# Kernel optimization log

Hardware: AMD Instinct MI355X
Metric: run time of the kernel (lower is better)

## Reference

```python
import jax, jax.numpy as jnp
import numpy as np

B, S, H = 4, 2048, 1024
NH, HD = 16, 64  # num heads, head dim


def setup_inputs() -> dict:
    key = jax.random.key(0)
    ks = jax.random.split(key, 8)
    s = 1.0 / np.sqrt(H)
    return {
        "hidden_states": jax.random.normal(ks[0], (B, S, H), jnp.float32),
        "attention_mask": jnp.zeros((B, 1, 1, S), jnp.float32),
        "Wq": jax.random.normal(ks[1], (H, H), jnp.float32) * s,
        "bq": jnp.zeros((H,), jnp.float32),
        "Wk": jax.random.normal(ks[2], (H, H), jnp.float32) * s,
        "bk": jnp.zeros((H,), jnp.float32),
        "Wv": jax.random.normal(ks[3], (H, H), jnp.float32) * s,
        "bv": jnp.zeros((H,), jnp.float32),
    }


def _split_heads(x):
    # [B, S, H] -> [B, NH, S, HD]
    return x.reshape(B, S, NH, HD).transpose(0, 2, 1, 3)


def reference(hidden_states, attention_mask, Wq, bq, Wk, bk, Wv, bv):
    q = _split_heads(hidden_states @ Wq + bq)
    k = _split_heads(hidden_states @ Wk + bk)
    v = _split_heads(hidden_states @ Wv + bv)
    scores = jnp.einsum("bhqd,bhkd->bhqk", q, k) / jnp.sqrt(jnp.float32(HD))
    probs = jax.nn.softmax(scores + attention_mask, axis=-1)  # dropout p=0 -> identity
    ctx = jnp.einsum("bhqk,bhkd->bhqd", probs, v)
    ctx = ctx.transpose(0, 2, 1, 3).reshape(B, S, H)
    return (ctx,)
```

## Files before the change

### kernel.cpp

```cpp
#include <hip/hip_runtime.h>
#include <hip/hip_bf16.h>
#include <stdint.h>


typedef unsigned short ushort_t;
typedef __attribute__((ext_vector_type(4))) float f32x4;
typedef __attribute__((ext_vector_type(16))) float f32x16;
typedef __attribute__((ext_vector_type(8))) short short8;

#define MFMA16(a, b, c) __builtin_amdgcn_mfma_f32_16x16x32_bf16((a), (b), (c), 0, 0, 0)
#define MFMA32(a, b, c) __builtin_amdgcn_mfma_f32_32x32x16_bf16((a), (b), (c), 0, 0, 0)

__device__ __forceinline__ ushort_t f2bf(float f) {
  unsigned u = __float_as_uint(f);
  u = (u + 0x7FFFu + ((u >> 16) & 1u)) >> 16;
  return (ushort_t)u;
}

typedef __attribute__((address_space(1))) unsigned int as1_uint;
typedef __attribute__((address_space(3))) unsigned int as3_uint;

__device__ __forceinline__ void async16(void* lds_dst, const void* g_src) {
  __builtin_amdgcn_global_load_lds((as1_uint*)(uintptr_t)g_src,
                                   (as3_uint*)(unsigned)(uintptr_t)lds_dst, 16, 0, 0);
}

__global__ __launch_bounds__(256) void convert_x(const float* __restrict__ X,
                                                 ushort_t* __restrict__ Xb) {
  int idx = (blockIdx.x * 256 + threadIdx.x) * 8;
  f32x4 a = *(const f32x4*)(X + idx);
  f32x4 b = *(const f32x4*)(X + idx + 4);
  short8 r;
#pragma unroll
  for (int j = 0; j < 4; ++j) r[j] = (short)f2bf(a[j]);
#pragma unroll
  for (int j = 0; j < 4; ++j) r[4 + j] = (short)f2bf(b[j]);
  *(short8*)(Xb + idx) = r;
}

__global__ __launch_bounds__(256) void convert_w(const float* __restrict__ Wq,
                                                 const float* __restrict__ Wk,
                                                 const float* __restrict__ Wv,
                                                 ushort_t* __restrict__ Wt) {
  const int mat = blockIdx.z;
  const float* W = (mat == 0) ? Wq : ((mat == 1) ? Wk : Wv);
  const int k0 = blockIdx.x * 64, n0 = blockIdx.y * 64;
  __shared__ float t[64][65];
  const int tid = threadIdx.x;
#pragma unroll
  for (int it = 0; it < 16; ++it) {
    int idx = it * 256 + tid;
    int r = idx >> 6, c = idx & 63;
    t[r][c] = W[(size_t)(k0 + r) * 1024 + n0 + c];
  }
  __syncthreads();
#pragma unroll
  for (int it = 0; it < 16; ++it) {
    int idx = it * 256 + tid;
    int nr = idx >> 6, kc = idx & 63;
    Wt[(size_t)(mat * 1024 + n0 + nr) * 1024 + k0 + kc] = f2bf(t[kc][nr]);
  }
}

__global__ __launch_bounds__(256) void gemm_qkv(const ushort_t* __restrict__ Xb,
                                                const ushort_t* __restrict__ Wt,
                                                const float* __restrict__ bq,
                                                const float* __restrict__ bk,
                                                const float* __restrict__ bv,
                                                ushort_t* __restrict__ Qb,
                                                ushort_t* __restrict__ Kb,
                                                ushort_t* __restrict__ Vt) {
  __shared__ char lds[36864];
  const int tid = threadIdx.x;
  const int l = tid & 63, w = tid >> 6;
  const int m0 = blockIdx.x * 128;
  const int n0 = blockIdx.y * 128;
  const int wm = w >> 1, wn = w & 1;

  const int lr = l >> 3;
  const int kb_log = (((l & 7) ^ lr) << 4);
  const char* srcA = (const char*)Xb + (size_t)(m0 + w * 32 + lr) * 2048 + kb_log;
  const char* srcB = (const char*)Wt + (size_t)(n0 + w * 32 + lr) * 2048 + kb_log;
  char* ldsA_w = lds + w * 4096;
  char* ldsB_w = lds + 16384 + w * 4096;

  const int ra = wm * 64 + (l & 15);
  const int rb = wn * 64 + (l & 15);
  const int swz = (l & 7) << 4;
  const int x0 = (((l >> 4) << 4)) ^ swz;
  const int x1 = (64 + ((l >> 4) << 4)) ^ swz;

  f32x4 acc[4][4];
#pragma unroll
  for (int mf = 0; mf < 4; ++mf)
#pragma unroll
    for (int nf = 0; nf < 4; ++nf) acc[mf][nf] = (f32x4){0.f, 0.f, 0.f, 0.f};

#pragma unroll 1
  for (int kt = 0; kt < 16; ++kt) {
    if (kt) __syncthreads();
    const int koff = kt * 128;
#pragma unroll
    for (int c = 0; c < 4; ++c) {
      async16(ldsA_w + c * 1024, srcA + c * 16384 + koff);
      async16(ldsB_w + c * 1024, srcB + c * 16384 + koff);
    }
    __syncthreads();
#pragma unroll
    for (int half = 0; half < 2; ++half) {
      const int xo = half ? x1 : x0;
      short8 av[4], bv2[4];
#pragma unroll
      for (int mf = 0; mf < 4; ++mf)
        av[mf] = *(const short8*)(lds + (ra + mf * 16) * 128 + xo);
#pragma unroll
      for (int nf = 0; nf < 4; ++nf)
        bv2[nf] = *(const short8*)(lds + 16384 + (rb + nf * 16) * 128 + xo);
#pragma unroll
      for (int mf = 0; mf < 4; ++mf)
#pragma unroll
        for (int nf = 0; nf < 4; ++nf)
          acc[mf][nf] = MFMA16(av[mf], bv2[nf], acc[mf][nf]);
    }
  }

  __syncthreads();
  const int col0 = n0 + wn * 64;
  const int mat = col0 >> 10;
  const int nn0 = col0 & 1023;
  const int hh = nn0 >> 6;
  const int row0 = m0 + wm * 64;
  const int bb = row0 >> 11;
  const int s0 = row0 & 2047;
  const float* bias = (mat == 0) ? bq : ((mat == 1) ? bk : bv);
  const float qscale = 0.18033688011112042f;
  if (mat < 2) {
    ushort_t* dst = (mat == 0) ? Qb : Kb;
    const float scl = (mat == 0) ? qscale : 1.0f;
#pragma unroll
    for (int mf = 0; mf < 4; ++mf)
#pragma unroll
      for (int nf = 0; nf < 4; ++nf)
#pragma unroll
        for (int i = 0; i < 4; ++i) {
          int r = mf * 16 + (l >> 4) * 4 + i;
          int d = nf * 16 + (l & 15);
          float v = (acc[mf][nf][i] + bias[nn0 + d]) * scl;
          dst[((size_t)(bb * 16 + hh) * 2048 + (s0 + r)) * 64 + d] = f2bf(v);
        }
  } else {
    ushort_t* vw = (ushort_t*)(lds + w * 9216);
#pragma unroll
    for (int mf = 0; mf < 4; ++mf)
#pragma unroll
      for (int nf = 0; nf < 4; ++nf)
#pragma unroll
        for (int i = 0; i < 4; ++i) {
          int r = mf * 16 + (l >> 4) * 4 + i;
          int d = nf * 16 + (l & 15);
          float v = acc[mf][nf][i] + bias[nn0 + d];
          vw[d * 72 + r] = f2bf(v);
        }
#pragma unroll
    for (int it = 0; it < 8; ++it) {
      int dr = it * 8 + (l >> 3);
      int sc = (l & 7) * 8;
      short8 vv = *(const short8*)((const char*)vw + dr * 144 + sc * 2);
      *(short8*)((char*)Vt + (((size_t)(bb * 16 + hh) * 64 + dr) * 2048 + s0 + sc) * 2) = vv;
    }
  }
}

__global__ __launch_bounds__(256, 4) void attn_fwd(const ushort_t* __restrict__ Qb,
                                                   const ushort_t* __restrict__ Kb,
                                                   const ushort_t* __restrict__ Vt,
                                                   const float* __restrict__ mask,
                                                   float* __restrict__ out) {
  __shared__ char lds[33280];
  const int tid = threadIdx.x, l = tid & 63, w = tid >> 6;
  const int bh = blockIdx.y;
  const int bb = bh >> 4, hh = bh & 15;
  const int q0 = blockIdx.x * 128;
  const int l31 = l & 31, hi = l >> 5;
  char* klds = lds;
  char* vlds = lds + 16384;
  float* sbuf = (float*)(lds + 32768) + w * 32;

  const float LOG2E = 1.44269504088896340736f;
  const int psz = (l & 7) << 4;

  const char* qrow = (const char*)Qb + ((size_t)bh * 2048 + q0 + w * 32 + l31) * 128 + hi * 16;
  short8 qf[4];
#pragma unroll
  for (int c = 0; c < 4; ++c) qf[c] = *(const short8*)(qrow + c * 32);

  const int srow = l >> 3;
  const int scol = ((l & 7) ^ srow) << 4;
  const char* ksrc0 = (const char*)Kb + (size_t)bh * 2048 * 128 + (size_t)(w * 16 + srow) * 128 + scol;
  const char* vsrc0 = (const char*)Vt + ((size_t)bh * 64 + w * 16 + srow) * 4096 + scol;

  {
    char* kd = klds + w * 2048;
    char* vd = vlds + w * 2048;
    async16(kd, ksrc0);
    async16(kd + 1024, ksrc0 + 1024);
    async16(vd, vsrc0);
    async16(vd + 1024, vsrc0 + 8 * 4096);
  }

  const float* mrow = mask + (size_t)bb * 2048;

  f32x16 o0, o1;
#pragma unroll
  for (int i = 0; i < 16; ++i) { o0[i] = 0.f; o1[i] = 0.f; }
  f32x4 lsum4 = (f32x4){0.f, 0.f, 0.f, 0.f};

#pragma unroll 1
  for (int kt = 0; kt < 32; ++kt) {
    const int cur = kt & 1;
    asm volatile("s_waitcnt lgkmcnt(0)" ::: "memory");
    __builtin_amdgcn_s_barrier();
    __builtin_amdgcn_sched_barrier(0);
    if (kt < 31) {
      char* kd = klds + (cur ^ 1) * 8192 + w * 2048;
      char* vd = vlds + (cur ^ 1) * 8192 + w * 2048;
      const char* ks = ksrc0 + (size_t)(kt + 1) * 8192;
      const char* vs = vsrc0 + (kt + 1) * 128;
      async16(kd, ks);
      async16(kd + 1024, ks + 1024);
      async16(vd, vs);
      async16(vd + 1024, vs + 8 * 4096);
      asm volatile("s_waitcnt vmcnt(4)" ::: "memory");
    } else {
      asm volatile("s_waitcnt vmcnt(0)" ::: "memory");
    }
    __builtin_amdgcn_s_barrier();
    __builtin_amdgcn_sched_barrier(0);

    const char* kbuf = klds + cur * 8192;
    const char* vbuf = vlds + cur * 8192;

#pragma unroll
    for (int kb = 0; kb < 2; ++kb) {
      f32x16 s;
#pragma unroll
      for (int i = 0; i < 16; ++i) s[i] = 0.f;
#pragma unroll
      for (int c = 0; c < 4; ++c) {
        short8 kf = *(const short8*)(kbuf + (kb * 32 + l31) * 128 + ((c * 32 + hi * 16) ^ psz));
        s = MFMA32(kf, qf[c], s);
      }
      f32x16 pp;
#pragma unroll
      for (int r2 = 0; r2 < 4; ++r2) {
        f32x4 m4 = *(const f32x4*)(mrow + kt * 64 + kb * 32 + 8 * r2 + 4 * hi);
#pragma unroll
        for (int i = 0; i < 4; ++i)
          pp[4 * r2 + i] = __builtin_amdgcn_exp2f(fmaf(m4[i], LOG2E, s[4 * r2 + i]));
      }
#pragma unroll
      for (int i = 0; i < 4; ++i)
        lsum4[i] += ((pp[i] + pp[4 + i]) + (pp[8 + i] + pp[12 + i]));

      unsigned u[8];
#pragma unroll
      for (int r2 = 0; r2 < 4; ++r2) {
        asm("v_cvt_pk_bf16_f32 %0, %1, %2"
            : "=v"(u[2 * r2]) : "v"(pp[4 * r2]), "v"(pp[4 * r2 + 1]));
        asm("v_cvt_pk_bf16_f32 %0, %1, %2"
            : "=v"(u[2 * r2 + 1]) : "v"(pp[4 * r2 + 2]), "v"(pp[4 * r2 + 3]));
      }
      short8 pa[2];
#pragma unroll
      for (int c = 0; c < 2; ++c) {
        unsigned a0 = u[4 * c], b0 = u[4 * c + 2];
        unsigned a1 = u[4 * c + 1], b1 = u[4 * c + 3];
        unsigned s0 = hi ? a0 : b0;
        unsigned s1 = hi ? a1 : b1;
        unsigned r0 = (unsigned)__shfl_xor((int)s0, 32);
        unsigned r1 = (unsigned)__shfl_xor((int)s1, 32);
        union { unsigned uu[4]; short8 s8; } cv;
        cv.uu[0] = hi ? r0 : a0;
        cv.uu[1] = hi ? r1 : a1;
        cv.uu[2] = hi ? b0 : r0;
        cv.uu[3] = hi ? b1 : r1;
        pa[c] = cv.s8;
      }

      __builtin_amdgcn_s_setprio(1);
#pragma unroll
      for (int c = 0; c < 2; ++c) {
        const int koff = (kb * 64 + c * 32 + hi * 16) ^ psz;
        short8 v0 = *(const short8*)(vbuf + l31 * 128 + koff);
        short8 v1 = *(const short8*)(vbuf + (32 + l31) * 128 + koff);
        o0 = MFMA32(pa[c], v0, o0);
        o1 = MFMA32(pa[c], v1, o1);
      }
      __builtin_amdgcn_s_setprio(0);
    }
  }

  float ls = (lsum4[0] + lsum4[1]) + (lsum4[2] + lsum4[3]);
  float other = __shfl_xor(ls, 32);
  float inv = 1.0f / (ls + other);
  if (hi == 0) sbuf[l31] = inv;
  float* obase = out + ((size_t)bb * 2048 + q0 + w * 32) * 1024 + hh * 64;
#pragma unroll
  for (int r2 = 0; r2 < 4; ++r2) {
    f32x4 iv = *(const f32x4*)(sbuf + 8 * r2 + 4 * hi);
#pragma unroll
    for (int r0 = 0; r0 < 4; ++r0) {
      const int q = 8 * r2 + 4 * hi + r0;
      obase[(size_t)q * 1024 + l31] = o0[4 * r2 + r0] * iv[r0];
      obase[(size_t)q * 1024 + 32 + l31] = o1[4 * r2 + r0] * iv[r0];
    }
  }
}

extern "C" void kernel_launch(void* const* d_in, const int* in_sizes, int n_in,
                              void* d_out, int out_size, void* d_ws, size_t ws_size,
                              hipStream_t stream) {
  const float* hs  = (const float*)d_in[0];
  const float* msk = (const float*)d_in[1];
  const float* Wq  = (const float*)d_in[2];
  const float* bq  = (const float*)d_in[3];
  const float* Wk  = (const float*)d_in[4];
  const float* bk  = (const float*)d_in[5];
  const float* Wv  = (const float*)d_in[6];
  const float* bv  = (const float*)d_in[7];
  float* out = (float*)d_out;
  char* ws = (char*)d_ws;
  ushort_t* Xb = (ushort_t*)ws;
  ushort_t* Wt = (ushort_t*)(ws + (16u << 20));
  ushort_t* Qb = (ushort_t*)(ws + (22u << 20));
  ushort_t* Kb = (ushort_t*)(ws + (38u << 20));
  ushort_t* Vt = (ushort_t*)(ws + (54u << 20));

  convert_x<<<4096, 256, 0, stream>>>(hs, Xb);
  convert_w<<<dim3(16, 16, 3), 256, 0, stream>>>(Wq, Wk, Wv, Wt);
  gemm_qkv<<<dim3(64, 24), 256, 0, stream>>>(Xb, Wt, bq, bk, bv, Qb, Kb, Vt);
  attn_fwd<<<dim3(16, 64), 256, 0, stream>>>(Qb, Kb, Vt, msk, out);
}
```

Before: 251.8 us.

## Rewrite QKV GEMM with 256x256 tiles and double-buffered async LDS pipeline

Enlarges the QKV projection GEMM tile from 128x128 with 4 waves to 256x256 with 8 waves, using a 128KB double-buffered LDS. Global-to-LDS async loads for the next K tile are interleaved with MFMA phases, using explicit waitcnt, barriers and s_setprio. The aim is to hide load latency and raise data reuse per block. In exchange, the large LDS footprint limits occupancy to one block per CU, and the 384-block grid may leave a partial last wave.

```diff
diff --git a/kernel.cpp b/kernel.cpp
--- a/kernel.cpp
+++ b/kernel.cpp
@@ -62,74 +62,154 @@
   }
 }
 
-__global__ __launch_bounds__(256) void gemm_qkv(const ushort_t* __restrict__ Xb,
-                                                const ushort_t* __restrict__ Wt,
-                                                const float* __restrict__ bq,
-                                                const float* __restrict__ bk,
-                                                const float* __restrict__ bv,
-                                                ushort_t* __restrict__ Qb,
-                                                ushort_t* __restrict__ Kb,
-                                                ushort_t* __restrict__ Vt) {
-  __shared__ char lds[36864];
+__global__ __launch_bounds__(512, 2) void gemm_qkv(const ushort_t* __restrict__ Xb,
+                                                   const ushort_t* __restrict__ Wt,
+                                                   const float* __restrict__ bq,
+                                                   const float* __restrict__ bk,
+                                                   const float* __restrict__ bv,
+                                                   ushort_t* __restrict__ Qb,
+                                                   ushort_t* __restrict__ Kb,
+                                                   ushort_t* __restrict__ Vt) {
+  __shared__ __align__(16) char lds[131072];
   const int tid = threadIdx.x;
   const int l = tid & 63, w = tid >> 6;
-  const int m0 = blockIdx.x * 128;
-  const int n0 = blockIdx.y * 128;
-  const int wm = w >> 1, wn = w & 1;
-
-  const int lr = l >> 3;
-  const int kb_log = (((l & 7) ^ lr) << 4);
-  const char* srcA = (const char*)Xb + (size_t)(m0 + w * 32 + lr) * 2048 + kb_log;
-  const char* srcB = (const char*)Wt + (size_t)(n0 + w * 32 + lr) * 2048 + kb_log;
-  char* ldsA_w = lds + w * 4096;
-  char* ldsB_w = lds + 16384 + w * 4096;
-
-  const int ra = wm * 64 + (l & 15);
-  const int rb = wn * 64 + (l & 15);
-  const int swz = (l & 7) << 4;
-  const int x0 = (((l >> 4) << 4)) ^ swz;
-  const int x1 = (64 + ((l >> 4) << 4)) ^ swz;
-
-  f32x4 acc[4][4];
-#pragma unroll
-  for (int mf = 0; mf < 4; ++mf)
+  const int wm = w >> 2, wn = w & 3;
+  const int m0 = blockIdx.x * 256;
+  const int n0 = blockIdx.y * 256;
+  const int l15 = l & 15, lg4 = l >> 4;
+  const int sw = (l & 7) << 4;
+
+  const int colb = (((l & 7) ^ (l >> 3)) << 4);
+  const char* srcA = (const char*)Xb + (size_t)(m0 + w * 16 + (l >> 3)) * 2048 + colb;
+  const char* srcB = (const char*)Wt + (size_t)(n0 + w * 16 + (l >> 3)) * 2048 + colb;
+  const int wrow = w * 16;
+
+#define STAGE(dst_base, src_base, h, t)                                     \
+  do {                                                                      \
+    const char* _g = (src_base) + (size_t)((h) * 128) * 2048 + (size_t)(t) * 128; \
+    char* _d = (dst_base) + (h) * 16384 + wrow * 128;                       \
+    async16(_d, _g);                                                        \
+    async16(_d + 1024, _g + 8 * 2048);                                      \
+  } while (0)
+
+  f32x4 acc[8][4];
+#pragma unroll
+  for (int mf = 0; mf < 8; ++mf)
 #pragma unroll
     for (int nf = 0; nf < 4; ++nf) acc[mf][nf] = (f32x4){0.f, 0.f, 0.f, 0.f};
 
+  STAGE(lds, srcA, 0, 0);
+  STAGE(lds, srcA, 1, 0);
+  STAGE(lds + 32768, srcB, 0, 0);
+  STAGE(lds + 32768, srcB, 1, 0);
+  STAGE(lds + 65536, srcA, 0, 1);
+  asm volatile("s_waitcnt vmcnt(2)" ::: "memory");
+  __builtin_amdgcn_s_barrier();
+  __builtin_amdgcn_sched_barrier(0);
+
+  short8 av[4][2], bv4[4][2];
+
 #pragma unroll 1
-  for (int kt = 0; kt < 16; ++kt) {
-    if (kt) __syncthreads();
-    const int koff = kt * 128;
-#pragma unroll
-    for (int c = 0; c < 4; ++c) {
-      async16(ldsA_w + c * 1024, srcA + c * 16384 + koff);
-      async16(ldsB_w + c * 1024, srcB + c * 16384 + koff);
+  for (int j = 0; j < 16; ++j) {
+    const char* sp = lds + (j & 1) * 65536;
+    char* os = lds + ((j & 1) ^ 1) * 65536;
+    char* cs = lds + (j & 1) * 65536;
+
+#pragma unroll
+    for (int mf = 0; mf < 4; ++mf)
+#pragma unroll
+      for (int kh = 0; kh < 2; ++kh)
+        av[mf][kh] = *(const short8*)(sp + (wm * 128 + mf * 16 + l15) * 128 +
+                                      (((kh * 4 + lg4) << 4) ^ sw));
+#pragma unroll
+    for (int nf = 0; nf < 2; ++nf)
+#pragma unroll
+      for (int kh = 0; kh < 2; ++kh)
+        bv4[nf][kh] = *(const short8*)(sp + 32768 + (wn * 64 + nf * 16 + l15) * 128 +
+                                       (((kh * 4 + lg4) << 4) ^ sw));
+    if (j < 15) STAGE(os, srcA, 1, j + 1);
+    __builtin_amdgcn_s_barrier();
+    asm volatile("s_waitcnt lgkmcnt(0)" ::: "memory");
+    __builtin_amdgcn_sched_barrier(0);
+    __builtin_amdgcn_s_setprio(1);
+#pragma unroll
+    for (int mf = 0; mf < 4; ++mf)
+#pragma unroll
+      for (int nf = 0; nf < 2; ++nf) {
+        acc[mf][nf] = MFMA16(av[mf][0], bv4[nf][0], acc[mf][nf]);
+        acc[mf][nf] = MFMA16(av[mf][1], bv4[nf][1], acc[mf][nf]);
+      }
+    __builtin_amdgcn_s_setprio(0);
+    __builtin_amdgcn_s_barrier();
+
+#pragma unroll
+    for (int nf = 0; nf < 2; ++nf)
+#pragma unroll
+      for (int kh = 0; kh < 2; ++kh)
+        bv4[2 + nf][kh] = *(const short8*)(sp + 32768 + (wn * 64 + (2 + nf) * 16 + l15) * 128 +
+                                           (((kh * 4 + lg4) << 4) ^ sw));
+    if (j < 15) STAGE(os + 32768, srcB, 0, j + 1);
+    __builtin_amdgcn_s_barrier();
+    asm volatile("s_waitcnt lgkmcnt(0)" ::: "memory");
+    __builtin_amdgcn_sched_barrier(0);
+    __builtin_amdgcn_s_setprio(1);
+#pragma unroll
+    for (int mf = 0; mf < 4; ++mf)
+#pragma unroll
+      for (int nf = 2; nf < 4; ++nf) {
+        acc[mf][nf] = MFMA16(av[mf][0], bv4[nf][0], acc[mf][nf]);
+        acc[mf][nf] = MFMA16(av[mf][1], bv4[nf][1], acc[mf][nf]);
+      }
+    __builtin_amdgcn_s_setprio(0);
+    __builtin_amdgcn_s_barrier();
+
+#pragma unroll
+    for (int mf = 0; mf < 4; ++mf)
+#pragma unroll
+      for (int kh = 0; kh < 2; ++kh)
+        av[mf][kh] = *(const short8*)(sp + (wm * 128 + (4 + mf) * 16 + l15) * 128 +
+                                      (((kh * 4 + lg4) << 4) ^ sw));
+    if (j < 15) STAGE(os + 32768, srcB, 1, j + 1);
+    __builtin_amdgcn_s_barrier();
+    asm volatile("s_waitcnt lgkmcnt(0)" ::: "memory");
+    __builtin_amdgcn_sched_barrier(0);
+    __builtin_amdgcn_s_setprio(1);
+#pragma unroll
+    for (int mf = 0; mf < 4; ++mf)
+#pragma unroll
+      for (int nf = 2; nf < 4; ++nf) {
+        acc[4 + mf][nf] = MFMA16(av[mf][0], bv4[nf][0], acc[4 + mf][nf]);
+        acc[4 + mf][nf] = MFMA16(av[mf][1], bv4[nf][1], acc[4 + mf][nf]);
+      }
+    __builtin_amdgcn_s_setprio(0);
+    __builtin_amdgcn_s_barrier();
+
+    if (j < 14) {
+      STAGE(cs, srcA, 0, j + 2);
+      asm volatile("s_waitcnt vmcnt(1)" ::: "memory");
+    } else if (j == 14) {
+      asm volatile("s_waitcnt vmcnt(0)" ::: "memory");
     }
-    __syncthreads();
-#pragma unroll
-    for (int half = 0; half < 2; ++half) {
-      const int xo = half ? x1 : x0;
-      short8 av[4], bv2[4];
-#pragma unroll
-      for (int mf = 0; mf < 4; ++mf)
-        av[mf] = *(const short8*)(lds + (ra + mf * 16) * 128 + xo);
-#pragma unroll
-      for (int nf = 0; nf < 4; ++nf)
-        bv2[nf] = *(const short8*)(lds + 16384 + (rb + nf * 16) * 128 + xo);
-#pragma unroll
-      for (int mf = 0; mf < 4; ++mf)
-#pragma unroll
-        for (int nf = 0; nf < 4; ++nf)
-          acc[mf][nf] = MFMA16(av[mf], bv2[nf], acc[mf][nf]);
-    }
-  }
-
-  __syncthreads();
+    __builtin_amdgcn_s_barrier();
+    __builtin_amdgcn_sched_barrier(0);
+    __builtin_amdgcn_s_setprio(1);
+#pragma unroll
+    for (int mf = 0; mf < 4; ++mf)
+#pragma unroll
+      for (int nf = 0; nf < 2; ++nf) {
+        acc[4 + mf][nf] = MFMA16(av[mf][0], bv4[nf][0], acc[4 + mf][nf]);
+        acc[4 + mf][nf] = MFMA16(av[mf][1], bv4[nf][1], acc[4 + mf][nf]);
+      }
+    __builtin_amdgcn_s_setprio(0);
+    __builtin_amdgcn_s_barrier();
+  }
+#undef STAGE
+
   const int col0 = n0 + wn * 64;
   const int mat = col0 >> 10;
   const int nn0 = col0 & 1023;
   const int hh = nn0 >> 6;
-  const int row0 = m0 + wm * 64;
+  const int row0 = m0 + wm * 128;
   const int bb = row0 >> 11;
   const int s0 = row0 & 2047;
   const float* bias = (mat == 0) ? bq : ((mat == 1) ? bk : bv);
@@ -138,35 +218,38 @@
     ushort_t* dst = (mat == 0) ? Qb : Kb;
     const float scl = (mat == 0) ? qscale : 1.0f;
 #pragma unroll
-    for (int mf = 0; mf < 4; ++mf)
+    for (int mf = 0; mf < 8; ++mf)
 #pragma unroll
       for (int nf = 0; nf < 4; ++nf)
 #pragma unroll
         for (int i = 0; i < 4; ++i) {
-          int r = mf * 16 + (l >> 4) * 4 + i;
-          int d = nf * 16 + (l & 15);
+          int r = mf * 16 + lg4 * 4 + i;
+          int d = nf * 16 + l15;
           float v = (acc[mf][nf][i] + bias[nn0 + d]) * scl;
           dst[((size_t)(bb * 16 + hh) * 2048 + (s0 + r)) * 64 + d] = f2bf(v);
         }
   } else {
     ushort_t* vw = (ushort_t*)(lds + w * 9216);
-#pragma unroll
-    for (int mf = 0; mf < 4; ++mf)
-#pragma unroll
-      for (int nf = 0; nf < 4; ++nf)
-#pragma unroll
-        for (int i = 0; i < 4; ++i) {
-          int r = mf * 16 + (l >> 4) * 4 + i;
-          int d = nf * 16 + (l & 15);
-          float v = acc[mf][nf][i] + bias[nn0 + d];
-          vw[d * 72 + r] = f2bf(v);
-        }
-#pragma unroll
-    for (int it = 0; it < 8; ++it) {
-      int dr = it * 8 + (l >> 3);
-      int sc = (l & 7) * 8;
-      short8 vv = *(const short8*)((const char*)vw + dr * 144 + sc * 2);
-      *(short8*)((char*)Vt + (((size_t)(bb * 16 + hh) * 64 + dr) * 2048 + s0 + sc) * 2) = vv;
+#pragma unroll 1
+    for (int rh = 0; rh < 2; ++rh) {
+#pragma unroll
+      for (int mf = 0; mf < 4; ++mf)
+#pragma unroll
+        for (int nf = 0; nf < 4; ++nf)
+#pragma unroll
+          for (int i = 0; i < 4; ++i) {
+            int rl = mf * 16 + lg4 * 4 + i;
+            int d = nf * 16 + l15;
+            float v = acc[rh * 4 + mf][nf][i] + bias[nn0 + d];
+            vw[d * 72 + rl] = f2bf(v);
+          }
+#pragma unroll
+      for (int it = 0; it < 8; ++it) {
+        int dr = it * 8 + (l >> 3);
+        int sc = (l & 7) * 8;
+        short8 vv = *(const short8*)((const char*)vw + dr * 144 + sc * 2);
+        *(short8*)((char*)Vt + (((size_t)(bb * 16 + hh) * 64 + dr) * 2048 + s0 + rh * 64 + sc) * 2) = vv;
+      }
     }
   }
 }
@@ -338,6 +421,6 @@
 
   convert_x<<<4096, 256, 0, stream>>>(hs, Xb);
   convert_w<<<dim3(16, 16, 3), 256, 0, stream>>>(Wq, Wk, Wv, Wt);
-  gemm_qkv<<<dim3(64, 24), 256, 0, stream>>>(Xb, Wt, bq, bk, bv, Qb, Kb, Vt);
+  gemm_qkv<<<dim3(32, 12), 512, 0, stream>>>(Xb, Wt, bq, bk, bv, Qb, Kb, Vt);
   attn_fwd<<<dim3(16, 64), 256, 0, stream>>>(Qb, Kb, Vt, msk, out);
 }
```

Result: slower. 308.8 us (+22.6%).
